# Performance work log

Hardware: AMD Instinct MI355X
Metric: run time of the kernel (lower is better)

The kernel has to match this reference:

```python
import jax, jax.numpy as jnp
import numpy as np

RATIO = 0.08  # self.ratio_3 (frozen parameter)
# kernel point k -> (dx, dy) = (k//3-1, k%3-1); matches torch.meshgrid('ij') flattening in offset_modulation
GX = np.repeat(np.arange(-1, 2), 3)  # [-1,-1,-1,0,0,0,1,1,1]
GY = np.tile(np.arange(-1, 2), 3)    # [-1,0,1,-1,0,1,-1,0,1]


def conv3(x, w, b):
    y = jax.lax.conv_general_dilated(x, w, (1, 1), ((1, 1), (1, 1)),
                                     dimension_numbers=('NCHW', 'OIHW', 'NCHW'))
    return y + b[None, :, None, None]


def offset_modulation(offset):
    B, C, H, W = offset.shape
    ov = offset.reshape(B, C // 2, 2, H, W)
    crop = ov[:, 3:12]                      # 9 (x,y) pairs
    oxy = jnp.concatenate([crop[:, :, 0], crop[:, :, 1]], axis=1) * RATIO  # [B,18,H,W]
    grid = jnp.concatenate([jnp.asarray(GX), jnp.asarray(GY)]).astype(offset.dtype)
    return oxy - grid[None, :, None, None]


def bilinear_sample(x, py, px):
    # x: [B,C,H,W]; py,px: [B,H,W] float sample coords; zero outside bounds
    B, C, H, W = x.shape
    y0 = jnp.floor(py); x0 = jnp.floor(px)
    wy = py - y0; wx = px - x0
    def gather(yi, xi):
        valid = ((yi >= 0) & (yi < H) & (xi >= 0) & (xi < W)).astype(x.dtype)
        yc = jnp.clip(yi, 0, H - 1).astype(jnp.int32)
        xc = jnp.clip(xi, 0, W - 1).astype(jnp.int32)
        g = jax.vmap(lambda img, yy, xx: img[:, yy, xx])(x, yc, xc)  # [B,C,H,W]
        return g * valid[:, None]
    return (gather(y0, x0) * ((1 - wy) * (1 - wx))[:, None]
            + gather(y0, x0 + 1) * ((1 - wy) * wx)[:, None]
            + gather(y0 + 1, x0) * (wy * (1 - wx))[:, None]
            + gather(y0 + 1, x0 + 1) * (wy * wx)[:, None])


def deform_conv(x, off, w, b):
    # off: [B,18,H,W], channels 0..8 = dx per kernel point, 9..17 = dy
    B, C, H, W = x.shape
    by = jnp.arange(H, dtype=x.dtype)[None, :, None]
    bx = jnp.arange(W, dtype=x.dtype)[None, None, :]
    out = jnp.zeros((B, w.shape[0], H, W), x.dtype)
    for k in range(9):
        py = by + GY[k] + off[:, 9 + k]
        px = bx + GX[k] + off[:, k]
        s = bilinear_sample(x, py, px)
        out = out + jnp.einsum('bchw,oc->bohw', s, w[:, :, GY[k] + 1, GX[k] + 1])
    return out + b[None, :, None, None]


def setup_inputs():
    key = jax.random.key(0)
    ks = iter(jax.random.split(key, 32))
    def p(*shape):
        return jax.random.normal(next(ks), shape, jnp.float32) * 0.05
    inp = {
        'x': jax.random.normal(next(ks), (2, 64, 256, 256), jnp.float32),
        'offset_0': jax.random.normal(next(ks), (2, 24, 256, 256), jnp.float32),
        'l12_w': p(64, 64, 3, 3), 'l12_b': p(64),
        'l13_w1': p(64, 64, 3, 3), 'l13_b1': p(64),
        'l13_w2': p(64, 64, 3, 3), 'l13_b2': p(64),
        'l14_w1': p(64, 64, 3, 3), 'l14_b1': p(64),
        'l14_w2': p(64, 64, 3, 3), 'l14_b2': p(64),
        'l15_w': p(32, 64, 3, 3), 'l15_b': p(32),
        'd50_w': p(32, 32, 3, 3), 'd50_b': p(32),
        'd51_w': p(32, 32, 3, 3), 'd51_b': p(32),
        'd60_w': p(32, 32, 3, 3), 'd60_b': p(32),
        'd61_w': p(32, 32, 3, 3), 'd61_b': p(32),
        'l24_w': p(3, 32, 3, 3), 'l24_b': p(3),
    }
    return inp


def reference(x, offset_0, l12_w, l12_b, l13_w1, l13_b1, l13_w2, l13_b2,
              l14_w1, l14_b1, l14_w2, l14_b2, l15_w, l15_b,
              d50_w, d50_b, d51_w, d51_b, d60_w, d60_b, d61_w, d61_b,
              l24_w, l24_b):
    off = offset_modulation(offset_0)
    x = conv3(x, l12_w, l12_b)
    x = conv3(jax.nn.relu(conv3(x, l13_w1, l13_b1)), l13_w2, l13_b2) + x
    x = conv3(jax.nn.relu(conv3(x, l14_w1, l14_b1)), l14_w2, l14_b2) + x
    x = conv3(x, l15_w, l15_b)
    r5 = jax.nn.relu(deform_conv(x, off, d50_w, d50_b))
    r5 = deform_conv(r5, off, d51_w, d51_b)
    x = x + r5
    r6 = jax.nn.relu(deform_conv(x, off, d60_w, d60_b))
    r6 = deform_conv(r6, off, d61_w, d61_b)
    x = x + r6
    return conv3(x, l24_w, l24_b)
```

## Files before the change

kernel.cpp:

```cpp
#include <hip/hip_runtime.h>

#define HH 256
#define WW 256
#define HW (HH * WW)

typedef float f32x4 __attribute__((ext_vector_type(4)));
typedef float f32x2 __attribute__((ext_vector_type(2)));
typedef short bf16x8 __attribute__((ext_vector_type(8)));

__device__ __forceinline__ unsigned short f2bf(float f) {
    union { float f; unsigned u; } v; v.f = f;
    unsigned r = v.u + 0x7fff + ((v.u >> 16) & 1);
    return (unsigned short)(r >> 16);
}
__device__ __forceinline__ float bflo(unsigned u) {
    union { unsigned u; float f; } v; v.u = u << 16; return v.f;
}
__device__ __forceinline__ float bfhi(unsigned u) {
    union { unsigned u; float f; } v; v.u = u & 0xffff0000u; return v.f;
}
__device__ __forceinline__ unsigned cvtpk(float lo, float hi) {
    unsigned r;
    asm("v_cvt_pk_bf16_f32 %0, %1, %2" : "=v"(r) : "v"(lo), "v"(hi));
    return r;
}
__device__ __forceinline__ f32x2 pkmul(f32x2 a, f32x2 b) {
    f32x2 d;
    asm("v_pk_mul_f32 %0, %1, %2" : "=v"(d) : "v"(a), "v"(b));
    return d;
}
__device__ __forceinline__ f32x2 pkfma(f32x2 a, f32x2 b, f32x2 c) {
    f32x2 d;
    asm("v_pk_fma_f32 %0, %1, %2, %3" : "=v"(d) : "v"(a), "v"(b), "v"(c));
    return d;
}
__device__ __forceinline__ f32x2 up2(unsigned u) {
    f32x2 r; 
    union { unsigned u; float f; } lo, hi;
    lo.u = u << 16; hi.u = u & 0xffff0000u;
    r[0] = lo.f; r[1] = hi.f;
    return r;
}

template <int W>
__device__ __forceinline__ bf16x8 lerp8(const unsigned short* __restrict__ tile,
                                        int lp, float wx, float wy, int kg) {
    const unsigned short* p = tile + lp * 40 + kg * 8;
    uint4 a00 = *(const uint4*)p;
    uint4 a01 = *(const uint4*)(p + 40);
    uint4 a10 = *(const uint4*)(p + W * 40);
    uint4 a11 = *(const uint4*)(p + W * 40 + 40);
    float omx = 1.f - wx, omy = 1.f - wy;
    float s00 = omy * omx, s01 = omy * wx, s10 = wy * omx, s11 = wy * wx;
    f32x2 w00p = {s00, s00}, w01p = {s01, s01}, w10p = {s10, s10}, w11p = {s11, s11};
    unsigned c00[4] = {a00.x, a00.y, a00.z, a00.w};
    unsigned c01[4] = {a01.x, a01.y, a01.z, a01.w};
    unsigned c10[4] = {a10.x, a10.y, a10.z, a10.w};
    unsigned c11[4] = {a11.x, a11.y, a11.z, a11.w};
    union { bf16x8 v; unsigned u[4]; } ur;
#pragma unroll
    for (int j = 0; j < 4; ++j) {
        f32x2 s = pkmul(w00p, up2(c00[j]));
        s = pkfma(w01p, up2(c01[j]), s);
        s = pkfma(w10p, up2(c10[j]), s);
        s = pkfma(w11p, up2(c11[j]), s);
        ur.u[j] = cvtpk(s[0], s[1]);
    }
    return ur.v;
}

__global__ void prepack_all(
    const float* w0, const float* w1, const float* w2, const float* w3,
    const float* w4, const float* w5, const float* w6, const float* w7,
    const float* w8, const float* w9,
    unsigned short* d0, unsigned short* d1, unsigned short* d2,
    unsigned short* d3, unsigned short* d4, unsigned short* d5,
    unsigned short* d6, unsigned short* d7, unsigned short* d8,
    unsigned short* d9) {
    const int L = blockIdx.y;
    const float* w; unsigned short* dst; int COUT, CIN;
    switch (L) {
        case 0: w = w0; dst = d0; COUT = 64; CIN = 64; break;
        case 1: w = w1; dst = d1; COUT = 64; CIN = 64; break;
        case 2: w = w2; dst = d2; COUT = 64; CIN = 64; break;
        case 3: w = w3; dst = d3; COUT = 64; CIN = 64; break;
        case 4: w = w4; dst = d4; COUT = 64; CIN = 64; break;
        case 5: w = w5; dst = d5; COUT = 32; CIN = 64; break;
        case 6: w = w6; dst = d6; COUT = 32; CIN = 32; break;
        case 7: w = w7; dst = d7; COUT = 32; CIN = 32; break;
        case 8: w = w8; dst = d8; COUT = 32; CIN = 32; break;
        default: w = w9; dst = d9; COUT = 32; CIN = 32; break;
    }
    int n = COUT * CIN * 9;
    int i = blockIdx.x * 256 + threadIdx.x;
    if (i >= n) return;
    int q = i & 31;
    int rest = i >> 5;
    int o = rest % COUT;
    int rest2 = rest / COUT;
    int KC = CIN >> 5;
    int kc = rest2 % KC;
    int t = rest2 / KC;
    int cin = kc * 32 + q;
    float v = w[((o * CIN + cin) * 3 + t / 3) * 3 + (t % 3)];
    dst[i] = f2bf(v);
}

template <bool SRCF32, int CIN, int COUT, bool RELU, bool ADDRES>
__global__ __launch_bounds__((COUT / 32) * 128) void convmfma(
    const void* __restrict__ in_, const unsigned short* __restrict__ wp,
    const float* __restrict__ bias, const unsigned short* __restrict__ res,
    unsigned short* __restrict__ out) {
    constexpr int KC = CIN / 32;
    constexpr int WM = COUT / 32;
    constexpr int NT = WM * 128;
    constexpr int CSTR = (CIN == 64) ? 72 : 40;
    __shared__ unsigned short xt[204 * CSTR];

    const int tid = threadIdx.x;
    const int b = blockIdx.z;
    const int bx0 = blockIdx.x * 32;
    const int by0 = blockIdx.y * 4;

    if (SRCF32) {
        const float* inb = (const float*)in_ + (size_t)b * CIN * HW;
        for (int hp = tid; hp < 204; hp += NT) {
            int hy = hp / 34, hx = hp - hy * 34;
            int gy = by0 + hy - 1, gx = bx0 + hx - 1;
            bool ok = ((unsigned)gy < HH) && ((unsigned)gx < WW);
            const float* src = inb + ((size_t)gy * WW + gx);
            unsigned* dstp = (unsigned*)&xt[hp * CSTR];
#pragma unroll 4
            for (int c = 0; c < CIN; c += 2) {
                float v0 = ok ? src[(size_t)c * HW] : 0.f;
                float v1 = ok ? src[(size_t)(c + 1) * HW] : 0.f;
                dstp[c >> 1] = cvtpk(v0, v1);
            }
        }
    } else {
        const unsigned short* inb = (const unsigned short*)in_ + (size_t)b * HW * CIN;
        constexpr int CH = CIN / 8;
        for (int idx = tid; idx < 204 * CH; idx += NT) {
            int hp = idx / CH, sub = idx - hp * CH;
            int hy = hp / 34, hx = hp - hy * 34;
            int gy = by0 + hy - 1, gx = bx0 + hx - 1;
            uint4 v = {0, 0, 0, 0};
            if (((unsigned)gy < HH) && ((unsigned)gx < WW))
                v = *(const uint4*)&inb[((size_t)gy * WW + gx) * CIN + sub * 8];
            *(uint4*)&xt[hp * CSTR + sub * 8] = v;
        }
    }
    __syncthreads();

    const int lane = tid & 63;
    const int wv = tid >> 6;
    const int wm = (WM == 2) ? (wv & 1) : 0;
    const int wn = (WM == 2) ? (wv >> 1) : wv;
    const int l15 = lane & 15;
    const int kg = lane >> 4;

    f32x4 acc[2][4];
#pragma unroll
    for (int m = 0; m < 2; ++m)
#pragma unroll
        for (int n = 0; n < 4; ++n) acc[m][n] = {0.f, 0.f, 0.f, 0.f};

    int hbase[4];
#pragma unroll
    for (int n = 0; n < 4; ++n) {
        int p = wn * 64 + n * 16 + l15;
        hbase[n] = (p >> 5) * 34 + (p & 31);
    }

    const unsigned short* wlane = wp + ((size_t)(wm * 32 + l15) * 4 + kg) * 8;

#pragma unroll
    for (int t = 0; t < 9; ++t) {
        bf16x8 afr[2][KC];
#pragma unroll
        for (int kc = 0; kc < KC; ++kc)
#pragma unroll
            for (int m = 0; m < 2; ++m)
                afr[m][kc] = *(const bf16x8*)(wlane + ((size_t)(t * KC + kc) * COUT + m * 16) * 32);

        const int hoff = (t / 3) * 34 + (t % 3);
#pragma unroll
        for (int kc = 0; kc < KC; ++kc) {
            bf16x8 bfr[4];
#pragma unroll
            for (int n = 0; n < 4; ++n)
                bfr[n] = *(const bf16x8*)&xt[(hbase[n] + hoff) * CSTR + kc * 32 + kg * 8];
#pragma unroll
            for (int m = 0; m < 2; ++m)
#pragma unroll
                for (int n = 0; n < 4; ++n)
                    acc[m][n] = __builtin_amdgcn_mfma_f32_16x16x32_bf16(afr[m][kc], bfr[n], acc[m][n], 0, 0, 0);
        }
    }

    const size_t pixbase = (size_t)b * HW;
#pragma unroll
    for (int m = 0; m < 2; ++m) {
#pragma unroll
        for (int n = 0; n < 4; ++n) {
            int p = wn * 64 + n * 16 + l15;
            int gy = by0 + (p >> 5), gx = bx0 + (p & 31);
            size_t pidx = (pixbase + (size_t)gy * WW + gx) * COUT;
            int cb = wm * 32 + m * 16 + kg * 4;
            float v[4];
#pragma unroll
            for (int r = 0; r < 4; ++r) {
                v[r] = acc[m][n][r] + bias[cb + r];
                if (RELU) v[r] = fmaxf(v[r], 0.f);
            }
            if (ADDRES) {
                uint2 rr = *(const uint2*)&res[pidx + cb];
                v[0] += bflo(rr.x); v[1] += bfhi(rr.x);
                v[2] += bflo(rr.y); v[3] += bfhi(rr.y);
            }
            uint2 o;
            o.x = cvtpk(v[0], v[1]);
            o.y = cvtpk(v[2], v[3]);
            *(uint2*)&out[pidx + cb] = o;
        }
    }
}

__global__ __launch_bounds__(512) void dpair(
    const unsigned short* __restrict__ in, const float* __restrict__ off0,
    const unsigned short* __restrict__ w1p, const float* __restrict__ b1,
    const unsigned short* __restrict__ w2p, const float* __restrict__ b2,
    unsigned short* __restrict__ out) {
    constexpr int CS = 40;
    __shared__ unsigned short xt[288 * CS];

    const int tid = threadIdx.x;
    const int b = blockIdx.z;
    const int bx0 = blockIdx.x * 32;
    const int by0 = blockIdx.y * 4;

    const unsigned short* inb = in + (size_t)b * HW * 32;
    for (int idx = tid; idx < 288 * 4; idx += 512) {
        int hp = idx >> 2, sub = idx & 3;
        int hy = hp / 36, hx = hp - hy * 36;
        int gy = by0 + hy - 2, gx = bx0 + hx - 2;
        uint4 v = {0, 0, 0, 0};
        if (((unsigned)gy < HH) && ((unsigned)gx < WW))
            v = *(const uint4*)&inb[((size_t)gy * WW + gx) * 32 + sub * 8];
        *(uint4*)&xt[hp * CS + sub * 8] = v;
    }
    __syncthreads();

    const int lane = tid & 63;
    const int wv = tid >> 6;
    const int l15 = lane & 15;
    const int kg = lane >> 4;
    const float* offB = off0 + (size_t)b * 24 * HW;

    f32x4 acc1[2][2];
#pragma unroll
    for (int m = 0; m < 2; ++m)
#pragma unroll
        for (int f = 0; f < 2; ++f) acc1[m][f] = {0.f, 0.f, 0.f, 0.f};

    int fgy[2], fgx[2], foff[2];
#pragma unroll
    for (int f = 0; f < 2; ++f) {
        int id = (wv * 2 + f) * 16 + l15;
        int rid = min(id, 203);
        int iy = rid / 34, ix = rid - iy * 34;
        fgy[f] = by0 - 1 + iy;
        fgx[f] = bx0 - 1 + ix;
        int cy = min(max(fgy[f], 0), HH - 1);
        int cx = min(max(fgx[f], 0), WW - 1);
        foff[f] = cy * WW + cx;
    }
    const unsigned short* w1l = w1p + (size_t)(l15 * 32 + kg * 8);

#pragma unroll 1
    for (int t = 0; t < 9; ++t) {
        const int k = (t % 3) * 3 + t / 3;
        const float* offx = offB + (size_t)(6 + 2 * k) * HW;
        const float* offy = offB + (size_t)(7 + 2 * k) * HW;
        bf16x8 afr[2];
#pragma unroll
        for (int m = 0; m < 2; ++m)
            afr[m] = *(const bf16x8*)(w1l + (size_t)(t * 32 + m * 16) * 32);

#pragma unroll
        for (int f = 0; f < 2; ++f) {
            if ((wv * 2 + f) * 16 >= 204) continue;
            float dxv = offx[foff[f]] * 0.08f;
            float dyv = offy[foff[f]] * 0.08f;
            float pxf = (float)fgx[f] + dxv;
            float pyf = (float)fgy[f] + dyv;
            float x0f = floorf(pxf), y0f = floorf(pyf);
            float wx = pxf - x0f, wy = pyf - y0f;
            int tx0 = min(max((int)x0f - (bx0 - 2), 0), 34);
            int ty0 = min(max((int)y0f - (by0 - 2), 0), 6);
            bf16x8 bfr = lerp8<36>(xt, ty0 * 36 + tx0, wx, wy, kg);
#pragma unroll
            for (int m = 0; m < 2; ++m)
                acc1[m][f] = __builtin_amdgcn_mfma_f32_16x16x32_bf16(afr[m], bfr, acc1[m][f], 0, 0, 0);
        }
    }
    __syncthreads();

#pragma unroll
    for (int f = 0; f < 2; ++f) {
        int id = (wv * 2 + f) * 16 + l15;
        bool ok = ((unsigned)fgy[f] < HH) && ((unsigned)fgx[f] < WW) && (id < 204);
#pragma unroll
        for (int m = 0; m < 2; ++m) {
            int cb = m * 16 + kg * 4;
            float v[4];
#pragma unroll
            for (int r = 0; r < 4; ++r)
                v[r] = ok ? fmaxf(acc1[m][f][r] + b1[cb + r], 0.f) : 0.f;
            uint2 o;
            o.x = cvtpk(v[0], v[1]);
            o.y = cvtpk(v[2], v[3]);
            *(uint2*)&xt[id * CS + cb] = o;
        }
    }
    __syncthreads();

    f32x4 acc2[2];
#pragma unroll
    for (int m = 0; m < 2; ++m) acc2[m] = {0.f, 0.f, 0.f, 0.f};

    const int py = by0 + (wv >> 1);
    const int pxb = bx0 + (wv & 1) * 16;
    const unsigned short* w2l = w2p + (size_t)(l15 * 32 + kg * 8);

#pragma unroll 1
    for (int t = 0; t < 9; ++t) {
        const int k = (t % 3) * 3 + t / 3;
        const float* offx = offB + (size_t)(6 + 2 * k) * HW + (size_t)py * WW;
        const float* offy = offB + (size_t)(7 + 2 * k) * HW + (size_t)py * WW;
        bf16x8 afr[2];
#pragma unroll
        for (int m = 0; m < 2; ++m)
            afr[m] = *(const bf16x8*)(w2l + (size_t)(t * 32 + m * 16) * 32);

        const int pxi = pxb + l15;
        float dxv = offx[pxi] * 0.08f;
        float dyv = offy[pxi] * 0.08f;
        float pxf = (float)pxi + dxv;
        float pyf = (float)py + dyv;
        float x0f = floorf(pxf), y0f = floorf(pyf);
        float wx = pxf - x0f, wy = pyf - y0f;
        int mx0 = min(max((int)x0f - (bx0 - 1), 0), 32);
        int my0 = min(max((int)y0f - (by0 - 1), 0), 4);
        bf16x8 bfr = lerp8<34>(xt, my0 * 34 + mx0, wx, wy, kg);
#pragma unroll
        for (int m = 0; m < 2; ++m)
            acc2[m] = __builtin_amdgcn_mfma_f32_16x16x32_bf16(afr[m], bfr, acc2[m], 0, 0, 0);
    }

    const int gx = pxb + l15;
    const size_t pidx = ((size_t)py * WW + gx) * 32;
    unsigned short* outb = out + (size_t)b * HW * 32;
#pragma unroll
    for (int m = 0; m < 2; ++m) {
        int cb = m * 16 + kg * 4;
        float v[4];
#pragma unroll
        for (int r = 0; r < 4; ++r) v[r] = acc2[m][r] + b2[cb + r];
        uint2 rr = *(const uint2*)&inb[pidx + cb];
        v[0] += bflo(rr.x); v[1] += bfhi(rr.x);
        v[2] += bflo(rr.y); v[3] += bfhi(rr.y);
        uint2 o;
        o.x = cvtpk(v[0], v[1]);
        o.y = cvtpk(v[2], v[3]);
        *(uint2*)&outb[pidx + cb] = o;
    }
}

__global__ __launch_bounds__(256) void conv3f(const unsigned short* __restrict__ in,
                                              const float* __restrict__ wgt,
                                              const float* __restrict__ bias,
                                              float* __restrict__ out) {
    __shared__ unsigned short xt[324 * 34];
    const int tid = threadIdx.x;
    const int lx = tid & 15, ly = tid >> 4;
    const int bx = blockIdx.x << 4, by = blockIdx.y << 4;
    const int b = blockIdx.z;

    const unsigned short* inb = in + (size_t)b * HW * 32;
    for (int idx = tid; idx < 324 * 8; idx += 256) {
        int hp = idx >> 3, sub = idx & 7;
        int hy = hp / 18, hx = hp - hy * 18;
        int gy = by + hy - 1, gx = bx + hx - 1;
        uint2 v = {0, 0};
        if (((unsigned)gy < HH) && ((unsigned)gx < WW))
            v = *(const uint2*)&inb[((size_t)gy * WW + gx) * 32 + sub * 4];
        *(uint2*)&xt[hp * 34 + sub * 4] = v;
    }
    __syncthreads();

    float a0 = bias[0], a1 = bias[1], a2 = bias[2];
#pragma unroll
    for (int ty = 0; ty < 3; ++ty) {
#pragma unroll
        for (int tx = 0; tx < 3; ++tx) {
            const unsigned short* row = &xt[((ly + ty) * 18 + lx + tx) * 34];
#pragma unroll 8
            for (int c = 0; c < 32; c += 2) {
                unsigned pv = *(const unsigned*)&row[c];
                float vl = bflo(pv), vh = bfhi(pv);
                const float* wl = wgt + (size_t)(c * 3 + ty) * 3 + tx;
                const float* whp = wgt + (size_t)((c + 1) * 3 + ty) * 3 + tx;
                a0 = fmaf(vl, wl[0], a0);          a0 = fmaf(vh, whp[0], a0);
                a1 = fmaf(vl, wl[32 * 9], a1);     a1 = fmaf(vh, whp[32 * 9], a1);
                a2 = fmaf(vl, wl[64 * 9], a2);     a2 = fmaf(vh, whp[64 * 9], a2);
            }
        }
    }
    const size_t o0 = ((size_t)b * 3) * HW + (size_t)(by + ly) * WW + bx + lx;
    out[o0] = a0;
    out[o0 + HW] = a1;
    out[o0 + 2 * HW] = a2;
}

extern "C" void kernel_launch(void* const* d_in, const int* in_sizes, int n_in,
                              void* d_out, int out_size, void* d_ws, size_t ws_size,
                              hipStream_t stream) {
    const float* x    = (const float*)d_in[0];
    const float* off0 = (const float*)d_in[1];
    const float* w12  = (const float*)d_in[2];
    const float* b12  = (const float*)d_in[3];
    const float* w13a = (const float*)d_in[4];
    const float* b13a = (const float*)d_in[5];
    const float* w13b = (const float*)d_in[6];
    const float* b13b = (const float*)d_in[7];
    const float* w14a = (const float*)d_in[8];
    const float* b14a = (const float*)d_in[9];
    const float* w14b = (const float*)d_in[10];
    const float* b14b = (const float*)d_in[11];
    const float* w15  = (const float*)d_in[12];
    const float* b15  = (const float*)d_in[13];
    const float* w50  = (const float*)d_in[14];
    const float* b50  = (const float*)d_in[15];
    const float* w51  = (const float*)d_in[16];
    const float* b51  = (const float*)d_in[17];
    const float* w60  = (const float*)d_in[18];
    const float* b60  = (const float*)d_in[19];
    const float* w61  = (const float*)d_in[20];
    const float* b61  = (const float*)d_in[21];
    const float* w24  = (const float*)d_in[22];
    const float* b24  = (const float*)d_in[23];

    unsigned short* A  = (unsigned short*)d_ws;
    unsigned short* Bb = A + (size_t)2 * HW * 64;
    unsigned short* D  = Bb;
    unsigned short* E  = Bb + (size_t)2 * HW * 32;
    unsigned short* wpk = Bb + (size_t)2 * HW * 64;
    const int SZ64 = 64 * 64 * 9;
    const int SZ32 = 32 * 64 * 9;
    const int SZD  = 32 * 32 * 9;
    unsigned short* p12  = wpk;
    unsigned short* p13a = p12 + SZ64;
    unsigned short* p13b = p13a + SZ64;
    unsigned short* p14a = p13b + SZ64;
    unsigned short* p14b = p14a + SZ64;
    unsigned short* p15  = p14b + SZ64;
    unsigned short* q50  = p15 + SZ32;
    unsigned short* q51  = q50 + SZD;
    unsigned short* q60  = q51 + SZD;
    unsigned short* q61  = q60 + SZD;
    float* out = (float*)d_out;

    prepack_all<<<dim3(144, 10), 256, 0, stream>>>(
        w12, w13a, w13b, w14a, w14b, w15, w50, w51, w60, w61,
        p12, p13a, p13b, p14a, p14b, p15, q50, q51, q60, q61);

    dim3 gm(WW / 32, HH / 4, 2);
    dim3 gd(WW / 32, HH / 4, 2);
    dim3 gs(HH / 16, WW / 16, 2);

    convmfma<true,  64, 64, false, false><<<gm, 256, 0, stream>>>(x,  p12,  b12,  nullptr, A);
    convmfma<false, 64, 64, true,  false><<<gm, 256, 0, stream>>>(A,  p13a, b13a, nullptr, Bb);
    convmfma<false, 64, 64, false, true ><<<gm, 256, 0, stream>>>(Bb, p13b, b13b, A, A);
    convmfma<false, 64, 64, true,  false><<<gm, 256, 0, stream>>>(A,  p14a, b14a, nullptr, Bb);
    convmfma<false, 64, 64, false, true ><<<gm, 256, 0, stream>>>(Bb, p14b, b14b, A, A);
    convmfma<false, 64, 32, false, false><<<gm, 128, 0, stream>>>(A,  p15,  b15,  nullptr, D);

    dpair<<<gd, 512, 0, stream>>>(D, off0, q50, b50, q51, b51, E);
    dpair<<<gd, 512, 0, stream>>>(E, off0, q60, b60, q61, b61, D);
    conv3f<<<gs, 256, 0, stream>>>(D, w24, b24, out);
}
```

Before: 236.5 us.

## Double dpair tile height to reduce halo recomputation in fused deform pair

Enlarges the fused deformable-conv pair tile from 4 to 8 output rows per block. The first deform conv then recomputes a smaller fraction of halo pixels (340 intermediates for 256 outputs versus 204 for 128). Each wave now handles three intermediate fragments and two output fragments, which raises register and LDS pressure. The grid shrinks to half as many blocks, which may reduce occupancy and parallelism.

Result: faster. 221.0 us (-6.5%).

```diff
diff --git a/kernel.cpp b/kernel.cpp
--- a/kernel.cpp
+++ b/kernel.cpp
@@ -35,7 +35,7 @@
     return d;
 }
 __device__ __forceinline__ f32x2 up2(unsigned u) {
-    f32x2 r; 
+    f32x2 r;
     union { unsigned u; float f; } lo, hi;
     lo.u = u << 16; hi.u = u & 0xffff0000u;
     r[0] = lo.f; r[1] = hi.f;
@@ -232,15 +232,15 @@
     const unsigned short* __restrict__ w2p, const float* __restrict__ b2,
     unsigned short* __restrict__ out) {
     constexpr int CS = 40;
-    __shared__ unsigned short xt[288 * CS];
+    __shared__ unsigned short xt[432 * CS];
 
     const int tid = threadIdx.x;
     const int b = blockIdx.z;
     const int bx0 = blockIdx.x * 32;
-    const int by0 = blockIdx.y * 4;
+    const int by0 = blockIdx.y * 8;
 
     const unsigned short* inb = in + (size_t)b * HW * 32;
-    for (int idx = tid; idx < 288 * 4; idx += 512) {
+    for (int idx = tid; idx < 432 * 4; idx += 512) {
         int hp = idx >> 2, sub = idx & 3;
         int hy = hp / 36, hx = hp - hy * 36;
         int gy = by0 + hy - 2, gx = bx0 + hx - 2;
@@ -257,17 +257,17 @@
     const int kg = lane >> 4;
     const float* offB = off0 + (size_t)b * 24 * HW;
 
-    f32x4 acc1[2][2];
+    f32x4 acc1[2][3];
 #pragma unroll
     for (int m = 0; m < 2; ++m)
 #pragma unroll
-        for (int f = 0; f < 2; ++f) acc1[m][f] = {0.f, 0.f, 0.f, 0.f};
-
-    int fgy[2], fgx[2], foff[2];
-#pragma unroll
-    for (int f = 0; f < 2; ++f) {
-        int id = (wv * 2 + f) * 16 + l15;
-        int rid = min(id, 203);
+        for (int f = 0; f < 3; ++f) acc1[m][f] = {0.f, 0.f, 0.f, 0.f};
+
+    int fgy[3], fgx[3], foff[3];
+#pragma unroll
+    for (int f = 0; f < 3; ++f) {
+        int id = (wv * 3 + f) * 16 + l15;
+        int rid = min(id, 339);
         int iy = rid / 34, ix = rid - iy * 34;
         fgy[f] = by0 - 1 + iy;
         fgx[f] = bx0 - 1 + ix;
@@ -288,8 +288,8 @@
             afr[m] = *(const bf16x8*)(w1l + (size_t)(t * 32 + m * 16) * 32);
 
 #pragma unroll
-        for (int f = 0; f < 2; ++f) {
-            if ((wv * 2 + f) * 16 >= 204) continue;
+        for (int f = 0; f < 3; ++f) {
+            if ((wv * 3 + f) * 16 >= 340) continue;
             float dxv = offx[foff[f]] * 0.08f;
             float dyv = offy[foff[f]] * 0.08f;
             float pxf = (float)fgx[f] + dxv;
@@ -297,7 +297,7 @@
             float x0f = floorf(pxf), y0f = floorf(pyf);
             float wx = pxf - x0f, wy = pyf - y0f;
             int tx0 = min(max((int)x0f - (bx0 - 2), 0), 34);
-            int ty0 = min(max((int)y0f - (by0 - 2), 0), 6);
+            int ty0 = min(max((int)y0f - (by0 - 2), 0), 10);
             bf16x8 bfr = lerp8<36>(xt, ty0 * 36 + tx0, wx, wy, kg);
 #pragma unroll
             for (int m = 0; m < 2; ++m)
@@ -307,9 +307,10 @@
     __syncthreads();
 
 #pragma unroll
-    for (int f = 0; f < 2; ++f) {
-        int id = (wv * 2 + f) * 16 + l15;
-        bool ok = ((unsigned)fgy[f] < HH) && ((unsigned)fgx[f] < WW) && (id < 204);
+    for (int f = 0; f < 3; ++f) {
+        int id = (wv * 3 + f) * 16 + l15;
+        bool ok = ((unsigned)fgy[f] < HH) && ((unsigned)fgx[f] < WW) && (id < 340);
+        int wid = min(id, 351);
 #pragma unroll
         for (int m = 0; m < 2; ++m) {
             int cb = m * 16 + kg * 4;
@@ -320,17 +321,18 @@
             uint2 o;
             o.x = cvtpk(v[0], v[1]);
             o.y = cvtpk(v[2], v[3]);
-            *(uint2*)&xt[id * CS + cb] = o;
+            *(uint2*)&xt[wid * CS + cb] = o;
         }
     }
     __syncthreads();
 
-    f32x4 acc2[2];
-#pragma unroll
-    for (int m = 0; m < 2; ++m) acc2[m] = {0.f, 0.f, 0.f, 0.f};
-
-    const int py = by0 + (wv >> 1);
-    const int pxb = bx0 + (wv & 1) * 16;
+    f32x4 acc2[2][2];
+#pragma unroll
+    for (int m = 0; m < 2; ++m)
+#pragma unroll
+        for (int n = 0; n < 2; ++n) acc2[m][n] = {0.f, 0.f, 0.f, 0.f};
+
+    const int py = by0 + wv;
     const unsigned short* w2l = w2p + (size_t)(l15 * 32 + kg * 8);
 
 #pragma unroll 1
@@ -343,37 +345,46 @@
         for (int m = 0; m < 2; ++m)
             afr[m] = *(const bf16x8*)(w2l + (size_t)(t * 32 + m * 16) * 32);
 
-        const int pxi = pxb + l15;
-        float dxv = offx[pxi] * 0.08f;
-        float dyv = offy[pxi] * 0.08f;
-        float pxf = (float)pxi + dxv;
-        float pyf = (float)py + dyv;
-        float x0f = floorf(pxf), y0f = floorf(pyf);
-        float wx = pxf - x0f, wy = pyf - y0f;
-        int mx0 = min(max((int)x0f - (bx0 - 1), 0), 32);
-        int my0 = min(max((int)y0f - (by0 - 1), 0), 4);
-        bf16x8 bfr = lerp8<34>(xt, my0 * 34 + mx0, wx, wy, kg);
+        bf16x8 bfr[2];
+#pragma unroll
+        for (int n = 0; n < 2; ++n) {
+            const int pxi = bx0 + n * 16 + l15;
+            float dxv = offx[pxi] * 0.08f;
+            float dyv = offy[pxi] * 0.08f;
+            float pxf = (float)pxi + dxv;
+            float pyf = (float)py + dyv;
+            float x0f = floorf(pxf), y0f = floorf(pyf);
+            float wx = pxf - x0f, wy = pyf - y0f;
+            int mx0 = min(max((int)x0f - (bx0 - 1), 0), 32);
+            int my0 = min(max((int)y0f - (by0 - 1), 0), 8);
+            bfr[n] = lerp8<34>(xt, my0 * 34 + mx0, wx, wy, kg);
+        }
 #pragma unroll
         for (int m = 0; m < 2; ++m)
-            acc2[m] = __builtin_amdgcn_mfma_f32_16x16x32_bf16(afr[m], bfr, acc2[m], 0, 0, 0);
-    }
-
-    const int gx = pxb + l15;
-    const size_t pidx = ((size_t)py * WW + gx) * 32;
+#pragma unroll
+            for (int n = 0; n < 2; ++n)
+                acc2[m][n] = __builtin_amdgcn_mfma_f32_16x16x32_bf16(afr[m], bfr[n], acc2[m][n], 0, 0, 0);
+    }
+
     unsigned short* outb = out + (size_t)b * HW * 32;
 #pragma unroll
-    for (int m = 0; m < 2; ++m) {
-        int cb = m * 16 + kg * 4;
-        float v[4];
-#pragma unroll
-        for (int r = 0; r < 4; ++r) v[r] = acc2[m][r] + b2[cb + r];
-        uint2 rr = *(const uint2*)&inb[pidx + cb];
-        v[0] += bflo(rr.x); v[1] += bfhi(rr.x);
-        v[2] += bflo(rr.y); v[3] += bfhi(rr.y);
-        uint2 o;
-        o.x = cvtpk(v[0], v[1]);
-        o.y = cvtpk(v[2], v[3]);
-        *(uint2*)&outb[pidx + cb] = o;
+    for (int n = 0; n < 2; ++n) {
+        int gx = bx0 + n * 16 + l15;
+        size_t pidx = ((size_t)py * WW + gx) * 32;
+#pragma unroll
+        for (int m = 0; m < 2; ++m) {
+            int cb = m * 16 + kg * 4;
+            float v[4];
+#pragma unroll
+            for (int r = 0; r < 4; ++r) v[r] = acc2[m][n][r] + b2[cb + r];
+            uint2 rr = *(const uint2*)&inb[pidx + cb];
+            v[0] += bflo(rr.x); v[1] += bfhi(rr.x);
+            v[2] += bflo(rr.y); v[3] += bfhi(rr.y);
+            uint2 o;
+            o.x = cvtpk(v[0], v[1]);
+            o.y = cvtpk(v[2], v[3]);
+            *(uint2*)&outb[pidx + cb] = o;
+        }
     }
 }
 
@@ -476,7 +487,7 @@
         p12, p13a, p13b, p14a, p14b, p15, q50, q51, q60, q61);
 
     dim3 gm(WW / 32, HH / 4, 2);
-    dim3 gd(WW / 32, HH / 4, 2);
+    dim3 gd(WW / 32, HH / 8, 2);
     dim3 gs(HH / 16, WW / 16, 2);
 
     convmfma<true,  64, 64, false, false><<<gm, 256, 0, stream>>>(x,  p12,  b12,  nullptr, A);
```
